# Performance work log

Measured on AMD Instinct MI355X. Metric: run time of the kernel, lower is better.

Reference implementation:

```python
import jax, jax.numpy as jnp
import numpy as np

B, S, H, A, F = 16, 512, 768, 12, 3072
DH = H // A  # 64
EPS = 1e-5

def layernorm(x, w, b):
    mu = jnp.mean(x, axis=-1, keepdims=True)
    var = jnp.mean(jnp.square(x - mu), axis=-1, keepdims=True)
    return (x - mu) * jax.lax.rsqrt(var + EPS) * w + b

def setup_inputs() -> dict:
    key = jax.random.key(0)
    ks = jax.random.split(key, 12)
    std = 0.02
    inp = {
        "X": jax.random.normal(ks[0], (B, S, H), jnp.float32),
        "mask": jax.random.randint(ks[1], (B, S), 0, 2, jnp.int32),
        "WQ": jax.random.normal(ks[2], (H, H), jnp.float32) * std,
        "bQ": jnp.zeros((H,), jnp.float32),
        "WK": jax.random.normal(ks[3], (H, H), jnp.float32) * std,
        "bK": jnp.zeros((H,), jnp.float32),
        "WV": jax.random.normal(ks[4], (H, H), jnp.float32) * std,
        "bV": jnp.zeros((H,), jnp.float32),
        "WO": jax.random.normal(ks[5], (H, H), jnp.float32) * std,
        "bO": jnp.zeros((H,), jnp.float32),
        "ln1_w": jnp.ones((H,), jnp.float32),
        "ln1_b": jnp.zeros((H,), jnp.float32),
        "W1": jax.random.normal(ks[6], (H, F), jnp.float32) * std,
        "b1": jnp.zeros((F,), jnp.float32),
        "W2": jax.random.normal(ks[7], (F, H), jnp.float32) * std,
        "b2": jnp.zeros((H,), jnp.float32),
        "ln2_w": jnp.ones((H,), jnp.float32),
        "ln2_b": jnp.zeros((H,), jnp.float32),
    }
    return inp

def reference(X, mask, WQ, bQ, WK, bK, WV, bV, WO, bO, ln1_w, ln1_b, W1, b1, W2, b2, ln2_w, ln2_b):
    # --- multi-head self-attention (pretrained-weights branch, faithful reshapes) ---
    Q = (X @ WQ + bQ).reshape(B, A, S, DH)
    K = (X @ WK + bK).reshape(B, A, S, DH)
    V = (X @ WV + bV).reshape(B, A, S, DH)
    scores = jnp.einsum('bhqd,bhkd->bhqk', Q, K) / jnp.sqrt(jnp.float32(DH))
    scores = jnp.where(mask[:, None, None, :] == 0, -jnp.inf, scores)
    attn = jax.nn.softmax(scores, axis=-1)
    Z = jnp.einsum('bhqk,bhkd->bhqd', attn, V).reshape(B, S, H)
    attn_out = Z @ WO + bO
    # residual + LN (dropout is identity in eval)
    X = layernorm(attn_out + X, ln1_w, ln1_b)
    # --- FFN with exact GELU ---
    ffn = jax.nn.gelu(X @ W1 + b1, approximate=False) @ W2 + b2
    X = layernorm(ffn + X, ln2_w, ln2_b)
    return X
```

## Files before the change

### kernel.cpp

```cpp
#include <hip/hip_runtime.h>
#include <hip/hip_bf16.h>


using bf16_t = __hip_bfloat16;
typedef __bf16 bf16x8 __attribute__((ext_vector_type(8)));
typedef float f32x4 __attribute__((ext_vector_type(4)));
typedef float f32x16 __attribute__((ext_vector_type(16)));

__device__ __forceinline__ float b2f(bf16_t v) { return __bfloat162float(v); }
__device__ __forceinline__ bf16_t f2b(float v) { return __float2bfloat16(v); }
__device__ __forceinline__ ushort f2bu(float v) { bf16_t b = f2b(v); return *(ushort*)&b; }

__device__ __forceinline__ void glds16(const ushort* g, ushort* l) {
    __builtin_amdgcn_global_load_lds(
        (const __attribute__((address_space(1))) unsigned int*)g,
        (__attribute__((address_space(3))) unsigned int*)l, 16, 0, 0);
}

__device__ __forceinline__ float gelu_f(float x) {
    float x2 = x * x;
    float y2 = 1.5957691216057308f * x * fmaf(0.044715f, x2, 1.0f);
    float e = __expf(y2);
    float t = 1.f - 2.f / (e + 1.f);
    return 0.5f * x * (1.f + t);
}

__device__ __forceinline__ void tr_tile(const float* __restrict__ in,
                                        bf16_t* __restrict__ out,
                                        int R, int C, int tx, int ty,
                                        float (*t)[65], int tid)
{
    int r0 = ty * 64, c0 = tx * 64;
    int tr = tid >> 6, tc = tid & 63;
#pragma unroll 4
    for (int i = 0; i < 16; ++i) {
        int r = i * 4 + tr;
        t[r][tc] = in[(size_t)(r0 + r) * C + c0 + tc];
    }
    __syncthreads();
#pragma unroll 4
    for (int i = 0; i < 16; ++i) {
        int r = i * 4 + tr;
        out[(size_t)(c0 + r) * R + r0 + tc] = f2b(t[tc][r]);
    }
}

__global__ __launch_bounds__(256) void prep_kernel(
    const float* __restrict__ WQ, const float* __restrict__ WK,
    const float* __restrict__ WV, const float* __restrict__ WO,
    const float* __restrict__ W1, const float* __restrict__ W2,
    const float* __restrict__ bQ, const float* __restrict__ bK,
    const float* __restrict__ bV, const float* __restrict__ X,
    bf16_t* __restrict__ Wqkv, bf16_t* __restrict__ WOt,
    bf16_t* __restrict__ W1t, bf16_t* __restrict__ W2t,
    float* __restrict__ bcat, bf16_t* __restrict__ Xb)
{
    __shared__ float t[64][65];
    const int blk = blockIdx.x, tid = threadIdx.x;
    if (blk < 576) {
        int m = blk / 144, tt = blk % 144;
        const float* in = (m == 0) ? WQ : (m == 1) ? WK : (m == 2) ? WV : WO;
        bf16_t* out = (m == 0) ? Wqkv : (m == 1) ? Wqkv + 589824
                    : (m == 2) ? Wqkv + 1179648 : WOt;
        tr_tile(in, out, 768, 768, tt % 12, tt / 12, t, tid);
    } else if (blk < 1152) {
        int tt = blk - 576;
        tr_tile(W1, W1t, 768, 3072, tt % 48, tt / 48, t, tid);
    } else if (blk < 1728) {
        int tt = blk - 1152;
        tr_tile(W2, W2t, 3072, 768, tt % 12, tt / 12, t, tid);
    } else if (blk == 1728) {
        for (int i = tid; i < 2304; i += 256)
            bcat[i] = (i < 768) ? bQ[i] : (i < 1536) ? bK[i - 768] : bV[i - 1536];
    } else {
        size_t i = ((size_t)(blk - 1729) * 256 + tid) * 8;
        float4 a = *(const float4*)(X + i);
        float4 b = *(const float4*)(X + i + 4);
#pragma unroll
        for (int j = 0; j < 4; ++j) {
            Xb[i + j]     = f2b(((const float*)&a)[j]);
            Xb[i + 4 + j] = f2b(((const float*)&b)[j]);
        }
    }
}

template <int EPI>
__global__ __launch_bounds__(512, 2) void gemm256(
    const bf16_t* __restrict__ A, const bf16_t* __restrict__ Bt,
    const float* __restrict__ bias, const void* __restrict__ res,
    void* __restrict__ Cv, int K, int lda, int ldb, int ldc)
{
    extern __shared__ ushort lds[];
    const int tid = threadIdx.x;
    const int l31 = tid & 31, khalf = (tid >> 5) & 1;
    const int w = tid >> 6;
    const int wr = w >> 2, wc = w & 3;
    const int m0 = blockIdx.x * 256, n0 = blockIdx.y * 256;

    const int srow = tid >> 3;
    const int sg = (((tid & 7) ^ (srow & 7)) << 3);
    const ushort* gA = (const ushort*)A + (size_t)(m0 + srow) * lda + sg;
    const ushort* gB = (const ushort*)Bt + (size_t)(n0 + srow) * ldb + sg;
    const int dOff = tid * 8;

    f32x16 acc[4][2] = {};
    const int arow = wr * 128, brow = wc * 64;
    const int nk = K >> 6;

#pragma unroll
    for (int p = 0; p < 4; ++p) {
        glds16(gA + (size_t)(p * 64) * lda, lds + p * 4096 + dOff);
        glds16(gB + (size_t)(p * 64) * ldb, lds + 16384 + p * 4096 + dOff);
    }
    asm volatile("s_waitcnt vmcnt(0)" ::: "memory");
    __builtin_amdgcn_s_barrier();

    for (int kt = 0; kt < nk; ++kt) {
        const int bo = (kt & 1) << 15;
        const ushort* sA = lds + bo;
        const ushort* sB = lds + bo + 16384;
        ushort* nA = lds + (bo ^ 32768);
        ushort* nB = lds + (bo ^ 32768) + 16384;
        const bool hasNext = (kt + 1) < nk;
        const size_t kn = (size_t)(kt + 1) << 6;
#pragma unroll
        for (int kk = 0; kk < 4; ++kk) {
            const int pc = (((kk * 2 + khalf) ^ (l31 & 7)) << 3);
            bf16x8 afr[4], bfr[2];
#pragma unroll
            for (int mi = 0; mi < 4; ++mi)
                afr[mi] = *(const bf16x8*)&sA[(arow + mi * 32 + l31) * 64 + pc];
#pragma unroll
            for (int ni = 0; ni < 2; ++ni)
                bfr[ni] = *(const bf16x8*)&sB[(brow + ni * 32 + l31) * 64 + pc];
            if (kk == 0 && hasNext) {
#pragma unroll
                for (int p = 0; p < 4; ++p)
                    glds16(gA + kn + (size_t)(p * 64) * lda, nA + p * 4096 + dOff);
            }
            if (kk == 1 && hasNext) {
#pragma unroll
                for (int p = 0; p < 4; ++p)
                    glds16(gB + kn + (size_t)(p * 64) * ldb, nB + p * 4096 + dOff);
            }
            __builtin_amdgcn_s_barrier();
            asm volatile("s_waitcnt lgkmcnt(0)" ::: "memory");
            __builtin_amdgcn_sched_barrier(0);
            __builtin_amdgcn_s_setprio(1);
#pragma unroll
            for (int mi = 0; mi < 4; ++mi)
#pragma unroll
                for (int ni = 0; ni < 2; ++ni)
                    acc[mi][ni] = __builtin_amdgcn_mfma_f32_32x32x16_bf16(bfr[ni], afr[mi], acc[mi][ni], 0, 0, 0);
            __builtin_amdgcn_s_setprio(0);
            if (kk == 3 && hasNext)
                asm volatile("s_waitcnt vmcnt(0)" ::: "memory");
            __builtin_amdgcn_s_barrier();
        }
    }

#pragma unroll
    for (int mi = 0; mi < 4; ++mi) {
        int m = m0 + arow + mi * 32 + l31;
#pragma unroll
        for (int ni = 0; ni < 2; ++ni) {
#pragma unroll
            for (int g = 0; g < 4; ++g) {
                int nb = n0 + brow + ni * 32 + 8 * g + 4 * khalf;
                float4 bv4 = *(const float4*)&bias[nb];
                float v[4];
#pragma unroll
                for (int r = 0; r < 4; ++r) v[r] = acc[mi][ni][g * 4 + r] + ((const float*)&bv4)[r];
                if constexpr (EPI == 1) {
#pragma unroll
                    for (int r = 0; r < 4; ++r) v[r] = gelu_f(v[r]);
                }
                ushort4 st;
                st.x = f2bu(v[0]); st.y = f2bu(v[1]); st.z = f2bu(v[2]); st.w = f2bu(v[3]);
                if constexpr (EPI == 6) {
                    int seg = n0 / 768;
                    int nloc = (n0 % 768) + brow + ni * 32 + 8 * g + 4 * khalf;
                    if (seg < 2) {
                        bf16_t* Cseg = (bf16_t*)Cv + (size_t)seg * 6291456;
                        *(ushort4*)&((ushort*)Cseg)[(size_t)m * 768 + nloc] = st;
                    } else {
                        ushort* vt = (ushort*)res;
                        int fb = (m & 511) * 768 + nloc;
                        int h = (m >> 9) * 12 + (fb >> 15);
                        int d = fb & 63;
                        int s = (fb >> 6) & 511;
                        ushort* vh = vt + (size_t)h * 32768 + s;
                        vh[(size_t)(d + 0) * 512] = st.x;
                        vh[(size_t)(d + 1) * 512] = st.y;
                        vh[(size_t)(d + 2) * 512] = st.z;
                        vh[(size_t)(d + 3) * 512] = st.w;
                    }
                } else {
                    *(ushort4*)&((ushort*)Cv)[(size_t)m * ldc + nb] = st;
                }
            }
        }
    }
}

template <int EPI, int NTILE>
__global__ __launch_bounds__(256) void gemm128(
    const bf16_t* __restrict__ A, const bf16_t* __restrict__ Bt,
    const float* __restrict__ bias, const void* __restrict__ res,
    void* __restrict__ Cv, int K, int lda, int ldb, int ldc)
{
    __shared__ ushort lA[128 * 64];
    __shared__ ushort lB[NTILE * 64];
    constexpr int NI = NTILE / 64;
    const int tid = threadIdx.x;
    const int l = tid & 63, w = tid >> 6;
    const int l31 = l & 31, khalf = l >> 5;
    const int m0 = blockIdx.x * 128, n0 = blockIdx.y * NTILE;

    const int srow = tid >> 3;
    const int sg = (((tid & 7) ^ (srow & 7)) << 3);
    const ushort* gA = (const ushort*)A + (size_t)(m0 + srow) * lda + sg;
    const ushort* gB = (const ushort*)Bt + (size_t)(n0 + srow) * ldb + sg;
    ushort* dA = lA + tid * 8;
    ushort* dB = lB + tid * 8;

    f32x16 acc[2][NI] = {};
    const int arow = (w & 1) * 64;
    const int brow = (w >> 1) * (NTILE / 2);

    for (int k0 = 0; k0 < K; k0 += 64) {
        __syncthreads();
        glds16(gA + k0,                      dA);
        glds16(gA + k0 + (size_t)32 * lda,   dA + 2048);
        glds16(gA + k0 + (size_t)64 * lda,   dA + 4096);
        glds16(gA + k0 + (size_t)96 * lda,   dA + 6144);
        glds16(gB + k0,                      dB);
        glds16(gB + k0 + (size_t)32 * ldb,   dB + 2048);
        if constexpr (NTILE == 128) {
            glds16(gB + k0 + (size_t)64 * ldb, dB + 4096);
            glds16(gB + k0 + (size_t)96 * ldb, dB + 6144);
        }
        __syncthreads();
#pragma unroll
        for (int kk = 0; kk < 4; ++kk) {
            const int pc = (((kk * 2 + khalf) ^ (l31 & 7)) << 3);
            bf16x8 bfr[NI];
#pragma unroll
            for (int ni = 0; ni < NI; ++ni)
                bfr[ni] = *(const bf16x8*)&lB[(brow + ni * 32 + l31) * 64 + pc];
#pragma unroll
            for (int mi = 0; mi < 2; ++mi) {
                bf16x8 afr = *(const bf16x8*)&lA[(arow + mi * 32 + l31) * 64 + pc];
#pragma unroll
                for (int ni = 0; ni < NI; ++ni)
                    acc[mi][ni] = __builtin_amdgcn_mfma_f32_32x32x16_bf16(bfr[ni], afr, acc[mi][ni], 0, 0, 0);
            }
        }
    }

#pragma unroll
    for (int mi = 0; mi < 2; ++mi) {
        int m = m0 + arow + mi * 32 + l31;
#pragma unroll
        for (int ni = 0; ni < NI; ++ni) {
#pragma unroll
            for (int g = 0; g < 4; ++g) {
                int nb = n0 + brow + ni * 32 + 8 * g + 4 * khalf;
                float4 bv4 = *(const float4*)&bias[nb];
                float v[4];
#pragma unroll
                for (int r = 0; r < 4; ++r) v[r] = acc[mi][ni][g * 4 + r] + ((const float*)&bv4)[r];
                if constexpr (EPI == 1) {
#pragma unroll
                    for (int r = 0; r < 4; ++r) v[r] = gelu_f(v[r]);
                } else if constexpr (EPI == 2) {
                    float4 r4 = *(const float4*)&((const float*)res)[(size_t)m * ldc + nb];
#pragma unroll
                    for (int r = 0; r < 4; ++r) v[r] += ((const float*)&r4)[r];
                } else if constexpr (EPI == 5) {
                    ushort4 rb = *(const ushort4*)&((const ushort*)res)[(size_t)m * ldc + nb];
#pragma unroll
                    for (int r = 0; r < 4; ++r) v[r] += b2f(*(const bf16_t*)&((const ushort*)&rb)[r]);
                }
                if constexpr (EPI == 5) {
                    *(float4*)&((float*)Cv)[(size_t)m * ldc + nb] = make_float4(v[0], v[1], v[2], v[3]);
                } else {
                    ushort4 st;
                    st.x = f2bu(v[0]); st.y = f2bu(v[1]); st.z = f2bu(v[2]); st.w = f2bu(v[3]);
                    if constexpr (EPI == 6) {
                        int seg = n0 / 768;
                        int nloc = (n0 % 768) + brow + ni * 32 + 8 * g + 4 * khalf;
                        if (seg < 2) {
                            bf16_t* Cseg = (bf16_t*)Cv + (size_t)seg * 6291456;
                            *(ushort4*)&((ushort*)Cseg)[(size_t)m * 768 + nloc] = st;
                        } else {
                            ushort* vt = (ushort*)res;
                            int fb = (m & 511) * 768 + nloc;
                            int h = (m >> 9) * 12 + (fb >> 15);
                            int d = fb & 63;
                            int s = (fb >> 6) & 511;
                            ushort* vh = vt + (size_t)h * 32768 + s;
                            vh[(size_t)(d + 0) * 512] = st.x;
                            vh[(size_t)(d + 1) * 512] = st.y;
                            vh[(size_t)(d + 2) * 512] = st.z;
                            vh[(size_t)(d + 3) * 512] = st.w;
                        }
                    } else {
                        *(ushort4*)&((ushort*)Cv)[(size_t)m * ldc + nb] = st;
                    }
                }
            }
        }
    }
}

__global__ __launch_bounds__(256) void flash_kernel(
    const bf16_t* __restrict__ Q, const bf16_t* __restrict__ Kx,
    const bf16_t* __restrict__ Vt, const int* __restrict__ mask,
    bf16_t* __restrict__ Z)
{
    __shared__ ushort lK[64 * 64];
    __shared__ ushort lV[64 * 64];
    __shared__ ushort lP[128 * 72];

    const int h = blockIdx.y;
    const int q0 = blockIdx.x * 128;
    const ushort* Qh = (const ushort*)Q + (size_t)h * 32768;
    const ushort* Kh = (const ushort*)Kx + (size_t)h * 32768;
    const ushort* Vh = (const ushort*)Vt + (size_t)h * 32768;
    const int* mk = mask + (h / 12) * 512;
    ushort* Zh = (ushort*)Z + (size_t)h * 32768;

    const int tid = threadIdx.x;
    const int l = tid & 63, w = tid >> 6;
    const int l16 = l & 15, quad = l >> 4;

    bf16x8 qfr[2][2];
#pragma unroll
    for (int mi = 0; mi < 2; ++mi)
#pragma unroll
        for (int kk = 0; kk < 2; ++kk)
            qfr[mi][kk] = *(const bf16x8*)(Qh + (size_t)(q0 + w * 32 + mi * 16 + l16) * 64 + kk * 32 + quad * 8);

    const int c8p = tid & 7;
    const int kr0 = tid >> 3;
    float m_i[2] = {-1e30f, -1e30f}, l_i[2] = {0.f, 0.f};
    f32x4 o4[2][4] = {};

    for (int kt = 0; kt < 8; ++kt) {
#pragma unroll
        for (int p = 0; p < 2; ++p) {
            int row = kr0 + p * 32;
            int c8l = c8p ^ (row & 7);
            glds16(Kh + (size_t)(kt * 64 + row) * 64 + c8l * 8, lK + (p * 256 + tid) * 8);
            glds16(Vh + (size_t)row * 512 + kt * 64 + c8l * 8, lV + (p * 256 + tid) * 8);
        }
        __syncthreads();

        f32x4 s4[2][4] = {};
#pragma unroll
        for (int kk = 0; kk < 2; ++kk) {
#pragma unroll
            for (int nt = 0; nt < 4; ++nt) {
                bf16x8 kfr = *(const bf16x8*)&lK[(nt * 16 + l16) * 64 + (((kk * 4 + quad) ^ (l16 & 7)) << 3)];
#pragma unroll
                for (int mi = 0; mi < 2; ++mi)
                    s4[mi][nt] = __builtin_amdgcn_mfma_f32_16x16x32_bf16(kfr, qfr[mi][kk], s4[mi][nt], 0, 0, 0);
            }
        }

        int4 m4[4];
#pragma unroll
        for (int nt = 0; nt < 4; ++nt) m4[nt] = *(const int4*)&mk[kt * 64 + nt * 16 + quad * 4];

#pragma unroll
        for (int mi = 0; mi < 2; ++mi) {
            float pv[4][4];
            float rm = -1e30f;
#pragma unroll
            for (int nt = 0; nt < 4; ++nt)
#pragma unroll
                for (int r = 0; r < 4; ++r) {
                    float v = (((const int*)&m4[nt])[r] == 0) ? -1e30f : s4[mi][nt][r] * 0.125f;
                    pv[nt][r] = v;
                    rm = fmaxf(rm, v);
                }
            rm = fmaxf(rm, __shfl_xor(rm, 16));
            rm = fmaxf(rm, __shfl_xor(rm, 32));
            float mn = fmaxf(m_i[mi], rm);
            float al = __expf(m_i[mi] - mn);
            float rs = 0.f;
#pragma unroll
            for (int nt = 0; nt < 4; ++nt)
#pragma unroll
                for (int r = 0; r < 4; ++r) {
                    float e = __expf(pv[nt][r] - mn);
                    pv[nt][r] = e;
                    rs += e;
                }
            rs += __shfl_xor(rs, 16);
            rs += __shfl_xor(rs, 32);
            l_i[mi] = l_i[mi] * al + rs;
            m_i[mi] = mn;
#pragma unroll
            for (int dt = 0; dt < 4; ++dt)
#pragma unroll
                for (int r = 0; r < 4; ++r) o4[mi][dt][r] *= al;

#pragma unroll
            for (int nt = 0; nt < 4; ++nt) {
                ushort4 st;
                st.x = f2bu(pv[nt][0]); st.y = f2bu(pv[nt][1]);
                st.z = f2bu(pv[nt][2]); st.w = f2bu(pv[nt][3]);
                *(ushort4*)&lP[(w * 32 + mi * 16 + l16) * 72 + nt * 16 + quad * 4] = st;
            }
        }
        __syncthreads();

#pragma unroll
        for (int kk = 0; kk < 2; ++kk) {
#pragma unroll
            for (int dt = 0; dt < 4; ++dt) {
                bf16x8 bvfr = *(const bf16x8*)&lV[(dt * 16 + l16) * 64 + (((kk * 4 + quad) ^ (l16 & 7)) << 3)];
#pragma unroll
                for (int mi = 0; mi < 2; ++mi) {
                    bf16x8 pafr = *(const bf16x8*)&lP[(w * 32 + mi * 16 + l16) * 72 + kk * 32 + quad * 8];
                    o4[mi][dt] = __builtin_amdgcn_mfma_f32_16x16x32_bf16(bvfr, pafr, o4[mi][dt], 0, 0, 0);
                }
            }
        }
        __syncthreads();
    }

#pragma unroll
    for (int mi = 0; mi < 2; ++mi) {
        float inv = 1.f / l_i[mi];
#pragma unroll
        for (int dt = 0; dt < 4; ++dt) {
            ushort4 st;
            st.x = f2bu(o4[mi][dt][0] * inv); st.y = f2bu(o4[mi][dt][1] * inv);
            st.z = f2bu(o4[mi][dt][2] * inv); st.w = f2bu(o4[mi][dt][3] * inv);
            *(ushort4*)&Zh[(size_t)(q0 + w * 32 + mi * 16 + l16) * 64 + dt * 16 + quad * 4] = st;
        }
    }
}

__device__ __forceinline__ float to_f(float v)  { return v; }
__device__ __forceinline__ float to_f(bf16_t v) { return b2f(v); }
__device__ __forceinline__ void from_f(float& d, float v)  { d = v; }
__device__ __forceinline__ void from_f(bf16_t& d, float v) { d = f2b(v); }

template <typename TI, typename TO>
__global__ __launch_bounds__(256) void layernorm_kernel(
    const TI* __restrict__ X, const float* __restrict__ w,
    const float* __restrict__ b, TO* __restrict__ out)
{
    const TI* x = X + (size_t)blockIdx.x * 768;
    TO* o = out + (size_t)blockIdx.x * 768;
    int t = threadIdx.x;
    float v[3];
    float s = 0.f, sq = 0.f;
#pragma unroll
    for (int i = 0; i < 3; ++i) {
        v[i] = to_f(x[t + i * 256]);
        s += v[i]; sq += v[i] * v[i];
    }
#pragma unroll
    for (int off = 32; off; off >>= 1) { s += __shfl_xor(s, off); sq += __shfl_xor(sq, off); }
    __shared__ float s1[4], s2[4];
    int wave = t >> 6, lane = t & 63;
    if (lane == 0) { s1[wave] = s; s2[wave] = sq; }
    __syncthreads();
    s  = s1[0] + s1[1] + s1[2] + s1[3];
    sq = s2[0] + s2[1] + s2[2] + s2[3];
    float mu  = s * (1.f / 768.f);
    float var = sq * (1.f / 768.f) - mu * mu;
    float rs  = rsqrtf(var + 1e-5f);
#pragma unroll
    for (int i = 0; i < 3; ++i)
        from_f(o[t + i * 256], (v[i] - mu) * rs * w[t + i * 256] + b[t + i * 256]);
}

extern "C" void kernel_launch(void* const* d_in, const int* in_sizes, int n_in,
                              void* d_out, int out_size, void* d_ws, size_t ws_size,
                              hipStream_t stream)
{
    const float* X    = (const float*)d_in[0];
    const int*   mask = (const int*)  d_in[1];
    const float* WQ   = (const float*)d_in[2];
    const float* bQ   = (const float*)d_in[3];
    const float* WK   = (const float*)d_in[4];
    const float* bK   = (const float*)d_in[5];
    const float* WV   = (const float*)d_in[6];
    const float* bV   = (const float*)d_in[7];
    const float* WO   = (const float*)d_in[8];
    const float* bO   = (const float*)d_in[9];
    const float* ln1w = (const float*)d_in[10];
    const float* ln1b = (const float*)d_in[11];
    const float* W1   = (const float*)d_in[12];
    const float* b1   = (const float*)d_in[13];
    const float* W2   = (const float*)d_in[14];
    const float* b2   = (const float*)d_in[15];
    const float* ln2w = (const float*)d_in[16];
    const float* ln2b = (const float*)d_in[17];
    float* out = (float*)d_out;

    bf16_t* ws   = (bf16_t*)d_ws;
    bf16_t* Wqkv = ws;
    bf16_t* WOt  = Wqkv + 1769472;
    bf16_t* W1t  = WOt + 589824;
    bf16_t* W2t  = W1t + 2359296;
    float*  bcat = (float*)(W2t + 2359296);
    bf16_t* Qb   = W2t + 2359296 + 4608;
    bf16_t* Kb   = Qb + 6291456;
    bf16_t* Vb   = Kb + 6291456;
    bf16_t* Xb   = Vb + 6291456;
    bf16_t* Vt   = Xb + 6291456;
    bf16_t* Zb = Qb;
    bf16_t* Y1 = Xb;
    bf16_t* X1 = Qb;
    bf16_t* Hb = Kb;

    (void)hipFuncSetAttribute(reinterpret_cast<const void*>(&gemm256<6>),
                              hipFuncAttributeMaxDynamicSharedMemorySize, 131072);
    (void)hipFuncSetAttribute(reinterpret_cast<const void*>(&gemm256<1>),
                              hipFuncAttributeMaxDynamicSharedMemorySize, 131072);

    prep_kernel<<<4801, 256, 0, stream>>>(WQ, WK, WV, WO, W1, W2, bQ, bK, bV, X,
                                          Wqkv, WOt, W1t, W2t, bcat, Xb);

    gemm256<6><<<dim3(32, 9), 512, 131072, stream>>>(Xb, Wqkv, bcat, Vt, Qb,
                                                     768, 768, 768, 768);

    flash_kernel<<<dim3(4, 192), 256, 0, stream>>>(Qb, Kb, Vt, mask, Zb);

    gemm128<2, 64><<<dim3(64, 12), 256, 0, stream>>>(Zb, WOt, bO, X, Y1,
                                                     768, 768, 768, 768);
    layernorm_kernel<bf16_t, bf16_t><<<8192, 256, 0, stream>>>(Y1, ln1w, ln1b, X1);

    gemm256<1><<<dim3(32, 12), 512, 131072, stream>>>(X1, W1t, b1, nullptr, Hb,
                                                      768, 768, 768, 3072);
    gemm128<5, 64><<<dim3(64, 12), 256, 0, stream>>>(Hb, W2t, b2, X1, out,
                                                     3072, 3072, 3072, 768);
    layernorm_kernel<float, float><<<8192, 256, 0, stream>>>(out, ln2w, ln2b, out);
}
```

Baseline: 402.3 us.

## Rework big GEMM into 256x128 tiles with triple-buffered LDS and XCD-aware block remap

Replaces the 256x256 double-buffered GEMM with a 256x128-tile kernel. It uses a three-stage LDS ring with a single barrier per K-tile, drops the per-kk barriers, and issues the next-next tile's global loads up front. Block IDs are remapped so consecutive tiles spread across the 8 XCDs, and grids double in N to keep enough workgroups. Occupancy drops to one block per CU (147KB LDS), and each block has less operand reuse per MFMA.

Result: slower. 438.2 us (+8.9%).

```diff
diff --git a/kernel.cpp b/kernel.cpp
--- a/kernel.cpp
+++ b/kernel.cpp
@@ -85,7 +85,7 @@
 }
 
 template <int EPI>
-__global__ __launch_bounds__(512, 2) void gemm256(
+__global__ __launch_bounds__(512, 1) void gemm_v3(
     const bf16_t* __restrict__ A, const bf16_t* __restrict__ Bt,
     const float* __restrict__ bias, const void* __restrict__ res,
     void* __restrict__ Cv, int K, int lda, int ldb, int ldc)
@@ -94,8 +94,16 @@
     const int tid = threadIdx.x;
     const int l31 = tid & 31, khalf = (tid >> 5) & 1;
     const int w = tid >> 6;
-    const int wr = w >> 2, wc = w & 3;
-    const int m0 = blockIdx.x * 256, n0 = blockIdx.y * 256;
+    const int wr = w >> 1, wc = w & 1;
+
+    int gx = gridDim.x;
+    int nwg = gx * gridDim.y;
+    int id = blockIdx.y * gx + blockIdx.x;
+    if ((nwg & 7) == 0) {
+        int cpx = nwg >> 3;
+        id = (id & 7) * cpx + (id >> 3);
+    }
+    const int m0 = (id % gx) * 256, n0 = (id / gx) * 128;
 
     const int srow = tid >> 3;
     const int sg = (((tid & 7) ^ (srow & 7)) << 3);
@@ -103,64 +111,55 @@
     const ushort* gB = (const ushort*)Bt + (size_t)(n0 + srow) * ldb + sg;
     const int dOff = tid * 8;
 
-    f32x16 acc[4][2] = {};
-    const int arow = wr * 128, brow = wc * 64;
+    f32x16 acc[2][2] = {};
+    const int arow = wr * 64, brow = wc * 64;
     const int nk = K >> 6;
 
-#pragma unroll
-    for (int p = 0; p < 4; ++p) {
-        glds16(gA + (size_t)(p * 64) * lda, lds + p * 4096 + dOff);
-        glds16(gB + (size_t)(p * 64) * ldb, lds + 16384 + p * 4096 + dOff);
-    }
-    asm volatile("s_waitcnt vmcnt(0)" ::: "memory");
+    ushort* b0 = lds;
+    ushort* b1 = lds + 24576;
+    ushort* b2 = lds + 49152;
+
+    auto STAGE = [&](int t, ushort* buf) {
+        const size_t ko = (size_t)t << 6;
+#pragma unroll
+        for (int p = 0; p < 4; ++p)
+            glds16(gA + ko + (size_t)(p * 64) * lda, buf + p * 4096 + dOff);
+#pragma unroll
+        for (int p = 0; p < 2; ++p)
+            glds16(gB + ko + (size_t)(p * 64) * ldb, buf + 16384 + p * 4096 + dOff);
+    };
+
+    STAGE(0, b0);
+    STAGE(1, b1);
+    asm volatile("s_waitcnt vmcnt(6)" ::: "memory");
     __builtin_amdgcn_s_barrier();
 
     for (int kt = 0; kt < nk; ++kt) {
-        const int bo = (kt & 1) << 15;
-        const ushort* sA = lds + bo;
-        const ushort* sB = lds + bo + 16384;
-        ushort* nA = lds + (bo ^ 32768);
-        ushort* nB = lds + (bo ^ 32768) + 16384;
-        const bool hasNext = (kt + 1) < nk;
-        const size_t kn = (size_t)(kt + 1) << 6;
+        if (kt + 2 < nk) STAGE(kt + 2, b2);
+        __builtin_amdgcn_s_setprio(1);
 #pragma unroll
         for (int kk = 0; kk < 4; ++kk) {
             const int pc = (((kk * 2 + khalf) ^ (l31 & 7)) << 3);
-            bf16x8 afr[4], bfr[2];
-#pragma unroll
-            for (int mi = 0; mi < 4; ++mi)
-                afr[mi] = *(const bf16x8*)&sA[(arow + mi * 32 + l31) * 64 + pc];
-#pragma unroll
-            for (int ni = 0; ni < 2; ++ni)
-                bfr[ni] = *(const bf16x8*)&sB[(brow + ni * 32 + l31) * 64 + pc];
-            if (kk == 0 && hasNext) {
-#pragma unroll
-                for (int p = 0; p < 4; ++p)
-                    glds16(gA + kn + (size_t)(p * 64) * lda, nA + p * 4096 + dOff);
-            }
-            if (kk == 1 && hasNext) {
-#pragma unroll
-                for (int p = 0; p < 4; ++p)
-                    glds16(gB + kn + (size_t)(p * 64) * ldb, nB + p * 4096 + dOff);
-            }
+            bf16x8 a0 = *(const bf16x8*)&b0[(arow + l31) * 64 + pc];
+            bf16x8 a1 = *(const bf16x8*)&b0[(arow + 32 + l31) * 64 + pc];
+            bf16x8 f0 = *(const bf16x8*)&b0[16384 + (brow + l31) * 64 + pc];
+            bf16x8 f1 = *(const bf16x8*)&b0[16384 + (brow + 32 + l31) * 64 + pc];
+            acc[0][0] = __builtin_amdgcn_mfma_f32_32x32x16_bf16(f0, a0, acc[0][0], 0, 0, 0);
+            acc[0][1] = __builtin_amdgcn_mfma_f32_32x32x16_bf16(f1, a0, acc[0][1], 0, 0, 0);
+            acc[1][0] = __builtin_amdgcn_mfma_f32_32x32x16_bf16(f0, a1, acc[1][0], 0, 0, 0);
+            acc[1][1] = __builtin_amdgcn_mfma_f32_32x32x16_bf16(f1, a1, acc[1][1], 0, 0, 0);
+        }
+        __builtin_amdgcn_s_setprio(0);
+        if (kt + 1 < nk) {
+            if (kt + 2 < nk) asm volatile("s_waitcnt vmcnt(6)" ::: "memory");
+            else             asm volatile("s_waitcnt vmcnt(0)" ::: "memory");
             __builtin_amdgcn_s_barrier();
-            asm volatile("s_waitcnt lgkmcnt(0)" ::: "memory");
-            __builtin_amdgcn_sched_barrier(0);
-            __builtin_amdgcn_s_setprio(1);
-#pragma unroll
-            for (int mi = 0; mi < 4; ++mi)
-#pragma unroll
-                for (int ni = 0; ni < 2; ++ni)
-                    acc[mi][ni] = __builtin_amdgcn_mfma_f32_32x32x16_bf16(bfr[ni], afr[mi], acc[mi][ni], 0, 0, 0);
-            __builtin_amdgcn_s_setprio(0);
-            if (kk == 3 && hasNext)
-                asm volatile("s_waitcnt vmcnt(0)" ::: "memory");
-            __builtin_amdgcn_s_barrier();
-        }
-    }
-
-#pragma unroll
-    for (int mi = 0; mi < 4; ++mi) {
+        }
+        ushort* t0 = b0; b0 = b1; b1 = b2; b2 = t0;
+    }
+
+#pragma unroll
+    for (int mi = 0; mi < 2; ++mi) {
         int m = m0 + arow + mi * 32 + l31;
 #pragma unroll
         for (int ni = 0; ni < 2; ++ni) {
@@ -521,16 +520,16 @@
     bf16_t* X1 = Qb;
     bf16_t* Hb = Kb;
 
-    (void)hipFuncSetAttribute(reinterpret_cast<const void*>(&gemm256<6>),
-                              hipFuncAttributeMaxDynamicSharedMemorySize, 131072);
-    (void)hipFuncSetAttribute(reinterpret_cast<const void*>(&gemm256<1>),
-                              hipFuncAttributeMaxDynamicSharedMemorySize, 131072);
+    (void)hipFuncSetAttribute(reinterpret_cast<const void*>(&gemm_v3<6>),
+                              hipFuncAttributeMaxDynamicSharedMemorySize, 147456);
+    (void)hipFuncSetAttribute(reinterpret_cast<const void*>(&gemm_v3<1>),
+                              hipFuncAttributeMaxDynamicSharedMemorySize, 147456);
 
     prep_kernel<<<4801, 256, 0, stream>>>(WQ, WK, WV, WO, W1, W2, bQ, bK, bV, X,
                                           Wqkv, WOt, W1t, W2t, bcat, Xb);
 
-    gemm256<6><<<dim3(32, 9), 512, 131072, stream>>>(Xb, Wqkv, bcat, Vt, Qb,
-                                                     768, 768, 768, 768);
+    gemm_v3<6><<<dim3(32, 18), 512, 147456, stream>>>(Xb, Wqkv, bcat, Vt, Qb,
+                                                      768, 768, 768, 768);
 
     flash_kernel<<<dim3(4, 192), 256, 0, stream>>>(Qb, Kb, Vt, mask, Zb);
 
@@ -538,7 +537,7 @@
                                                      768, 768, 768, 768);
     layernorm_kernel<bf16_t, bf16_t><<<8192, 256, 0, stream>>>(Y1, ln1w, ln1b, X1);
 
-    gemm256<1><<<dim3(32, 12), 512, 131072, stream>>>(X1, W1t, b1, nullptr, Hb,
+    gemm_v3<1><<<dim3(32, 24), 512, 147456, stream>>>(X1, W1t, b1, nullptr, Hb,
                                                       768, 768, 768, 3072);
     gemm128<5, 64><<<dim3(64, 12), 256, 0, stream>>>(Hb, W2t, b2, X1, out,
                                                      3072, 3072, 3072, 768);
```

## Rework 256x256 GEMM into 4-stage 32-wide K pipeline and use it for WO projection

Applied to the files above, without the earlier changes.

The 256x256 GEMM now loads 32-wide K slices combining A and B tiles into one 16K-element stage, keeping three stages in flight across a four-buffer ring. This replaces the double-buffered 64-wide K loop that had per-substep barriers, with one barrier per K step. Launch bounds drop to one block per CU, and the kernel gains a residual-add epilogue so the output projection runs on the large-tile kernel (96 blocks) instead of gemm128 (768 blocks). That risks poor CU utilisation for the WO GEMM. The dead EPI==6 branch is also removed from the gemm128 epilogue.

After: 417.2 us. +3.7%, slower.

```diff
diff --git a/kernel.cpp b/kernel.cpp
--- a/kernel.cpp
+++ b/kernel.cpp
@@ -85,7 +85,7 @@
 }
 
 template <int EPI>
-__global__ __launch_bounds__(512, 2) void gemm256(
+__global__ __launch_bounds__(512, 1) void gemm_v4(
     const bf16_t* __restrict__ A, const bf16_t* __restrict__ Bt,
     const float* __restrict__ bias, const void* __restrict__ res,
     void* __restrict__ Cv, int K, int lda, int ldb, int ldc)
@@ -97,66 +97,60 @@
     const int wr = w >> 2, wc = w & 3;
     const int m0 = blockIdx.x * 256, n0 = blockIdx.y * 256;
 
-    const int srow = tid >> 3;
-    const int sg = (((tid & 7) ^ (srow & 7)) << 3);
-    const ushort* gA = (const ushort*)A + (size_t)(m0 + srow) * lda + sg;
-    const ushort* gB = (const ushort*)Bt + (size_t)(n0 + srow) * ldb + sg;
+    const ushort* src[4];
+#pragma unroll
+    for (int p = 0; p < 4; ++p) {
+        int row = p * 64 + (tid >> 3);
+        int clog = (tid & 7) ^ (row & 7);
+        src[p] = (clog < 4)
+            ? (const ushort*)A  + (size_t)(m0 + row) * lda + clog * 8
+            : (const ushort*)Bt + (size_t)(n0 + row) * ldb + (clog - 4) * 8;
+    }
     const int dOff = tid * 8;
+
+    auto STAGE = [&](int t, ushort* buf) {
+        const int ko = t << 5;
+#pragma unroll
+        for (int p = 0; p < 4; ++p)
+            glds16(src[p] + ko, buf + p * 4096 + dOff);
+    };
 
     f32x16 acc[4][2] = {};
     const int arow = wr * 128, brow = wc * 64;
-    const int nk = K >> 6;
-
-#pragma unroll
-    for (int p = 0; p < 4; ++p) {
-        glds16(gA + (size_t)(p * 64) * lda, lds + p * 4096 + dOff);
-        glds16(gB + (size_t)(p * 64) * ldb, lds + 16384 + p * 4096 + dOff);
-    }
-    asm volatile("s_waitcnt vmcnt(0)" ::: "memory");
+    const int nk = K >> 5;
+
+    STAGE(0, lds);
+    STAGE(1, lds + 16384);
+    STAGE(2, lds + 32768);
+    asm volatile("s_waitcnt vmcnt(8)" ::: "memory");
     __builtin_amdgcn_s_barrier();
 
     for (int kt = 0; kt < nk; ++kt) {
-        const int bo = (kt & 1) << 15;
-        const ushort* sA = lds + bo;
-        const ushort* sB = lds + bo + 16384;
-        ushort* nA = lds + (bo ^ 32768);
-        ushort* nB = lds + (bo ^ 32768) + 16384;
-        const bool hasNext = (kt + 1) < nk;
-        const size_t kn = (size_t)(kt + 1) << 6;
-#pragma unroll
-        for (int kk = 0; kk < 4; ++kk) {
-            const int pc = (((kk * 2 + khalf) ^ (l31 & 7)) << 3);
+        if (kt + 3 < nk) STAGE(kt + 3, lds + ((kt + 3) & 3) * 16384);
+        const ushort* bt = lds + (kt & 3) * 16384;
+        __builtin_amdgcn_s_setprio(1);
+#pragma unroll
+        for (int kk = 0; kk < 2; ++kk) {
+            const int ca = (((kk * 2 + khalf)     ^ (l31 & 7)) << 3);
+            const int cb = (((4 + kk * 2 + khalf) ^ (l31 & 7)) << 3);
             bf16x8 afr[4], bfr[2];
 #pragma unroll
             for (int mi = 0; mi < 4; ++mi)
-                afr[mi] = *(const bf16x8*)&sA[(arow + mi * 32 + l31) * 64 + pc];
+                afr[mi] = *(const bf16x8*)&bt[(arow + mi * 32 + l31) * 64 + ca];
 #pragma unroll
             for (int ni = 0; ni < 2; ++ni)
-                bfr[ni] = *(const bf16x8*)&sB[(brow + ni * 32 + l31) * 64 + pc];
-            if (kk == 0 && hasNext) {
-#pragma unroll
-                for (int p = 0; p < 4; ++p)
-                    glds16(gA + kn + (size_t)(p * 64) * lda, nA + p * 4096 + dOff);
-            }
-            if (kk == 1 && hasNext) {
-#pragma unroll
-                for (int p = 0; p < 4; ++p)
-                    glds16(gB + kn + (size_t)(p * 64) * ldb, nB + p * 4096 + dOff);
-            }
-            __builtin_amdgcn_s_barrier();
-            asm volatile("s_waitcnt lgkmcnt(0)" ::: "memory");
-            __builtin_amdgcn_sched_barrier(0);
-            __builtin_amdgcn_s_setprio(1);
+                bfr[ni] = *(const bf16x8*)&bt[(brow + ni * 32 + l31) * 64 + cb];
 #pragma unroll
             for (int mi = 0; mi < 4; ++mi)
 #pragma unroll
                 for (int ni = 0; ni < 2; ++ni)
                     acc[mi][ni] = __builtin_amdgcn_mfma_f32_32x32x16_bf16(bfr[ni], afr[mi], acc[mi][ni], 0, 0, 0);
-            __builtin_amdgcn_s_setprio(0);
-            if (kk == 3 && hasNext)
-                asm volatile("s_waitcnt vmcnt(0)" ::: "memory");
-            __builtin_amdgcn_s_barrier();
-        }
+        }
+        __builtin_amdgcn_s_setprio(0);
+        if (kt + 3 < nk)      asm volatile("s_waitcnt vmcnt(8)" ::: "memory");
+        else if (kt + 2 < nk) asm volatile("s_waitcnt vmcnt(4)" ::: "memory");
+        else if (kt + 1 < nk) asm volatile("s_waitcnt vmcnt(0)" ::: "memory");
+        if (kt + 1 < nk) __builtin_amdgcn_s_barrier();
     }
 
 #pragma unroll
@@ -174,6 +168,10 @@
                 if constexpr (EPI == 1) {
 #pragma unroll
                     for (int r = 0; r < 4; ++r) v[r] = gelu_f(v[r]);
+                } else if constexpr (EPI == 2) {
+                    float4 r4 = *(const float4*)&((const float*)res)[(size_t)m * ldc + nb];
+#pragma unroll
+                    for (int r = 0; r < 4; ++r) v[r] += ((const float*)&r4)[r];
                 }
                 ushort4 st;
                 st.x = f2bu(v[0]); st.y = f2bu(v[1]); st.z = f2bu(v[2]); st.w = f2bu(v[3]);
@@ -287,27 +285,7 @@
                 } else {
                     ushort4 st;
                     st.x = f2bu(v[0]); st.y = f2bu(v[1]); st.z = f2bu(v[2]); st.w = f2bu(v[3]);
-                    if constexpr (EPI == 6) {
-                        int seg = n0 / 768;
-                        int nloc = (n0 % 768) + brow + ni * 32 + 8 * g + 4 * khalf;
-                        if (seg < 2) {
-                            bf16_t* Cseg = (bf16_t*)Cv + (size_t)seg * 6291456;
-                            *(ushort4*)&((ushort*)Cseg)[(size_t)m * 768 + nloc] = st;
-                        } else {
-                            ushort* vt = (ushort*)res;
-                            int fb = (m & 511) * 768 + nloc;
-                            int h = (m >> 9) * 12 + (fb >> 15);
-                            int d = fb & 63;
-                            int s = (fb >> 6) & 511;
-                            ushort* vh = vt + (size_t)h * 32768 + s;
-                            vh[(size_t)(d + 0) * 512] = st.x;
-                            vh[(size_t)(d + 1) * 512] = st.y;
-                            vh[(size_t)(d + 2) * 512] = st.z;
-                            vh[(size_t)(d + 3) * 512] = st.w;
-                        }
-                    } else {
-                        *(ushort4*)&((ushort*)Cv)[(size_t)m * ldc + nb] = st;
-                    }
+                    *(ushort4*)&((ushort*)Cv)[(size_t)m * ldc + nb] = st;
                 }
             }
         }
@@ -521,24 +499,26 @@
     bf16_t* X1 = Qb;
     bf16_t* Hb = Kb;
 
-    (void)hipFuncSetAttribute(reinterpret_cast<const void*>(&gemm256<6>),
+    (void)hipFuncSetAttribute(reinterpret_cast<const void*>(&gemm_v4<6>),
                               hipFuncAttributeMaxDynamicSharedMemorySize, 131072);
-    (void)hipFuncSetAttribute(reinterpret_cast<const void*>(&gemm256<1>),
+    (void)hipFuncSetAttribute(reinterpret_cast<const void*>(&gemm_v4<2>),
+                              hipFuncAttributeMaxDynamicSharedMemorySize, 131072);
+    (void)hipFuncSetAttribute(reinterpret_cast<const void*>(&gemm_v4<1>),
                               hipFuncAttributeMaxDynamicSharedMemorySize, 131072);
 
     prep_kernel<<<4801, 256, 0, stream>>>(WQ, WK, WV, WO, W1, W2, bQ, bK, bV, X,
                                           Wqkv, WOt, W1t, W2t, bcat, Xb);
 
-    gemm256<6><<<dim3(32, 9), 512, 131072, stream>>>(Xb, Wqkv, bcat, Vt, Qb,
+    gemm_v4<6><<<dim3(32, 9), 512, 131072, stream>>>(Xb, Wqkv, bcat, Vt, Qb,
                                                      768, 768, 768, 768);
 
     flash_kernel<<<dim3(4, 192), 256, 0, stream>>>(Qb, Kb, Vt, mask, Zb);
 
-    gemm128<2, 64><<<dim3(64, 12), 256, 0, stream>>>(Zb, WOt, bO, X, Y1,
+    gemm_v4<2><<<dim3(32, 3), 512, 131072, stream>>>(Zb, WOt, bO, X, Y1,
                                                      768, 768, 768, 768);
     layernorm_kernel<bf16_t, bf16_t><<<8192, 256, 0, stream>>>(Y1, ln1w, ln1b, X1);
 
-    gemm256<1><<<dim3(32, 12), 512, 131072, stream>>>(X1, W1t, b1, nullptr, Hb,
+    gemm_v4<1><<<dim3(32, 12), 512, 131072, stream>>>(X1, W1t, b1, nullptr, Hb,
                                                       768, 768, 768, 3072);
     gemm128<5, 64><<<dim3(64, 12), 256, 0, stream>>>(Hb, W2t, b2, X1, out,
                                                      3072, 3072, 3072, 768);
```

## Restructure 256-tile GEMM into two-phase prefetch loop and move QKV to 128-tile GEMM

Applied to the files above, without the earlier changes.

The 256x256 GEMM main loop changes from an interleaved schedule to a simple two-phase loop. The old loop issued A and B prefetches inside the k-substeps, with barriers and lgkm waits around every MFMA group. The new loop issues the whole next-tile prefetch up front, computes the current tile, then does one vmcnt wait and one barrier per k-tile. The launch bound drops to one block per SM, and the fused QKV scatter epilogue is removed from this kernel. The QKV projection now runs on the 128-row gemm128 kernel with a 128-wide N tile. The aim is to cut barrier overhead and get better grid balance for QKV, at the cost of less fine-grained load/compute interleaving.

Result: faster. 371.8 us (-7.6%).

```diff
diff --git a/kernel.cpp b/kernel.cpp
--- a/kernel.cpp
+++ b/kernel.cpp
@@ -85,7 +85,7 @@
 }
 
 template <int EPI>
-__global__ __launch_bounds__(512, 2) void gemm256(
+__global__ __launch_bounds__(512, 1) void gemm_2ph(
     const bf16_t* __restrict__ A, const bf16_t* __restrict__ Bt,
     const float* __restrict__ bias, const void* __restrict__ res,
     void* __restrict__ Cv, int K, int lda, int ldb, int ldc)
@@ -107,57 +107,53 @@
     const int arow = wr * 128, brow = wc * 64;
     const int nk = K >> 6;
 
-#pragma unroll
-    for (int p = 0; p < 4; ++p) {
-        glds16(gA + (size_t)(p * 64) * lda, lds + p * 4096 + dOff);
-        glds16(gB + (size_t)(p * 64) * ldb, lds + 16384 + p * 4096 + dOff);
-    }
-    asm volatile("s_waitcnt vmcnt(0)" ::: "memory");
-    __builtin_amdgcn_s_barrier();
-
-    for (int kt = 0; kt < nk; ++kt) {
-        const int bo = (kt & 1) << 15;
-        const ushort* sA = lds + bo;
-        const ushort* sB = lds + bo + 16384;
-        ushort* nA = lds + (bo ^ 32768);
-        ushort* nB = lds + (bo ^ 32768) + 16384;
-        const bool hasNext = (kt + 1) < nk;
-        const size_t kn = (size_t)(kt + 1) << 6;
+    STAGE_DEF:;
+    auto STAGE = [&](int t, int cur) {
+        ushort* buf = lds + cur * 32768;
+        const size_t ko = (size_t)t << 6;
+#pragma unroll
+        for (int p = 0; p < 4; ++p)
+            glds16(gA + ko + (size_t)(p * 64) * lda, buf + p * 4096 + dOff);
+#pragma unroll
+        for (int p = 0; p < 4; ++p)
+            glds16(gB + ko + (size_t)(p * 64) * ldb, buf + 16384 + p * 4096 + dOff);
+    };
+
+    auto COMPUTE = [&](int cur) {
+        const ushort* buf = lds + cur * 32768;
 #pragma unroll
         for (int kk = 0; kk < 4; ++kk) {
             const int pc = (((kk * 2 + khalf) ^ (l31 & 7)) << 3);
             bf16x8 afr[4], bfr[2];
 #pragma unroll
             for (int mi = 0; mi < 4; ++mi)
-                afr[mi] = *(const bf16x8*)&sA[(arow + mi * 32 + l31) * 64 + pc];
+                afr[mi] = *(const bf16x8*)&buf[(arow + mi * 32 + l31) * 64 + pc];
 #pragma unroll
             for (int ni = 0; ni < 2; ++ni)
-                bfr[ni] = *(const bf16x8*)&sB[(brow + ni * 32 + l31) * 64 + pc];
-            if (kk == 0 && hasNext) {
-#pragma unroll
-                for (int p = 0; p < 4; ++p)
-                    glds16(gA + kn + (size_t)(p * 64) * lda, nA + p * 4096 + dOff);
-            }
-            if (kk == 1 && hasNext) {
-#pragma unroll
-                for (int p = 0; p < 4; ++p)
-                    glds16(gB + kn + (size_t)(p * 64) * ldb, nB + p * 4096 + dOff);
-            }
-            __builtin_amdgcn_s_barrier();
-            asm volatile("s_waitcnt lgkmcnt(0)" ::: "memory");
-            __builtin_amdgcn_sched_barrier(0);
-            __builtin_amdgcn_s_setprio(1);
+                bfr[ni] = *(const bf16x8*)&buf[16384 + (brow + ni * 32 + l31) * 64 + pc];
 #pragma unroll
             for (int mi = 0; mi < 4; ++mi)
 #pragma unroll
                 for (int ni = 0; ni < 2; ++ni)
                     acc[mi][ni] = __builtin_amdgcn_mfma_f32_32x32x16_bf16(bfr[ni], afr[mi], acc[mi][ni], 0, 0, 0);
-            __builtin_amdgcn_s_setprio(0);
-            if (kk == 3 && hasNext)
-                asm volatile("s_waitcnt vmcnt(0)" ::: "memory");
-            __builtin_amdgcn_s_barrier();
-        }
-    }
+        }
+    };
+
+    STAGE(0, 0);
+    asm volatile("s_waitcnt vmcnt(0)" ::: "memory");
+    __builtin_amdgcn_s_barrier();
+
+    int cur = 0;
+    for (int t = 0; t < nk - 1; ++t) {
+        STAGE(t + 1, cur ^ 1);
+        __builtin_amdgcn_s_setprio(1);
+        COMPUTE(cur);
+        __builtin_amdgcn_s_setprio(0);
+        asm volatile("s_waitcnt vmcnt(0)" ::: "memory");
+        __builtin_amdgcn_s_barrier();
+        cur ^= 1;
+    }
+    COMPUTE(cur);
 
 #pragma unroll
     for (int mi = 0; mi < 4; ++mi) {
@@ -177,27 +173,7 @@
                 }
                 ushort4 st;
                 st.x = f2bu(v[0]); st.y = f2bu(v[1]); st.z = f2bu(v[2]); st.w = f2bu(v[3]);
-                if constexpr (EPI == 6) {
-                    int seg = n0 / 768;
-                    int nloc = (n0 % 768) + brow + ni * 32 + 8 * g + 4 * khalf;
-                    if (seg < 2) {
-                        bf16_t* Cseg = (bf16_t*)Cv + (size_t)seg * 6291456;
-                        *(ushort4*)&((ushort*)Cseg)[(size_t)m * 768 + nloc] = st;
-                    } else {
-                        ushort* vt = (ushort*)res;
-                        int fb = (m & 511) * 768 + nloc;
-                        int h = (m >> 9) * 12 + (fb >> 15);
-                        int d = fb & 63;
-                        int s = (fb >> 6) & 511;
-                        ushort* vh = vt + (size_t)h * 32768 + s;
-                        vh[(size_t)(d + 0) * 512] = st.x;
-                        vh[(size_t)(d + 1) * 512] = st.y;
-                        vh[(size_t)(d + 2) * 512] = st.z;
-                        vh[(size_t)(d + 3) * 512] = st.w;
-                    }
-                } else {
-                    *(ushort4*)&((ushort*)Cv)[(size_t)m * ldc + nb] = st;
-                }
+                *(ushort4*)&((ushort*)Cv)[(size_t)m * ldc + nb] = st;
             }
         }
     }
@@ -521,16 +497,14 @@
     bf16_t* X1 = Qb;
     bf16_t* Hb = Kb;
 
-    (void)hipFuncSetAttribute(reinterpret_cast<const void*>(&gemm256<6>),
-                              hipFuncAttributeMaxDynamicSharedMemorySize, 131072);
-    (void)hipFuncSetAttribute(reinterpret_cast<const void*>(&gemm256<1>),
+    (void)hipFuncSetAttribute(reinterpret_cast<const void*>(&gemm_2ph<1>),
                               hipFuncAttributeMaxDynamicSharedMemorySize, 131072);
 
     prep_kernel<<<4801, 256, 0, stream>>>(WQ, WK, WV, WO, W1, W2, bQ, bK, bV, X,
                                           Wqkv, WOt, W1t, W2t, bcat, Xb);
 
-    gemm256<6><<<dim3(32, 9), 512, 131072, stream>>>(Xb, Wqkv, bcat, Vt, Qb,
-                                                     768, 768, 768, 768);
+    gemm128<6, 128><<<dim3(64, 18), 256, 0, stream>>>(Xb, Wqkv, bcat, Vt, Qb,
+                                                      768, 768, 768, 768);
 
     flash_kernel<<<dim3(4, 192), 256, 0, stream>>>(Qb, Kb, Vt, mask, Zb);
 
@@ -538,8 +512,8 @@
                                                      768, 768, 768, 768);
     layernorm_kernel<bf16_t, bf16_t><<<8192, 256, 0, stream>>>(Y1, ln1w, ln1b, X1);
 
-    gemm256<1><<<dim3(32, 12), 512, 131072, stream>>>(X1, W1t, b1, nullptr, Hb,
-                                                      768, 768, 768, 3072);
+    gemm_2ph<1><<<dim3(32, 12), 512, 131072, stream>>>(X1, W1t, b1, nullptr, Hb,
+                                                       768, 768, 768, 3072);
     gemm128<5, 64><<<dim3(64, 12), 256, 0, stream>>>(Hb, W2t, b2, X1, out,
                                                      3072, 3072, 3072, 768);
     layernorm_kernel<float, float><<<8192, 256, 0, stream>>>(out, ln2w, ln2b, out);
```
